# Kernel tuning notes

Measured on AMD Instinct MI355X. Metric: run time of the kernel, lower is better.

## Reference

```python
import jax, jax.numpy as jnp
import numpy as np

E = 250000          # num_edges
T = 1500000         # num_triplets
H = 128             # hidden_dim
NB = 8              # num_bilinear
NS = 7              # num_spherical
NR = 6              # num_radial
OUT = 128           # output_dim


def silu(x):
    return x * jax.nn.sigmoid(x)


def setup_inputs() -> dict:
    key = jax.random.key(0)
    ks = jax.random.split(key, 24)
    s = 1.0 / np.sqrt(H)
    inp = {
        "x": jax.random.normal(ks[0], (E, H), jnp.float32),
        "rbf": jax.random.uniform(ks[1], (E, NR), jnp.float32),
        "sbf": jax.random.uniform(ks[2], (T, NS * NR), jnp.float32),
        "idx_kj": jax.random.randint(ks[3], (T,), 0, E, jnp.int32),
        "idx_ji": jax.random.randint(ks[4], (T,), 0, E, jnp.int32),
        # weights stored [in, out] (math identical to torch y = x @ W.T + b)
        "lin_rbf_w": jax.random.normal(ks[5], (NR, H), jnp.float32) * (1.0 / np.sqrt(NR)),
        "lin_sbf_w": jax.random.normal(ks[6], (NS * NR, NB), jnp.float32) * (1.0 / np.sqrt(NS * NR)),
        "lin_kj_w": jax.random.normal(ks[7], (H, H), jnp.float32) * s,
        "lin_kj_b": jnp.zeros((H,), jnp.float32),
        "lin_ji_w": jax.random.normal(ks[8], (H, H), jnp.float32) * s,
        "lin_ji_b": jnp.zeros((H,), jnp.float32),
        "W": jax.random.normal(ks[9], (H, NB, H), jnp.float32) * (2.0 / H),
        "rb_w1": jax.random.normal(ks[10], (H, H), jnp.float32) * s,
        "rb_b1": jnp.zeros((H,), jnp.float32),
        "rb_w2": jax.random.normal(ks[11], (H, H), jnp.float32) * s,
        "rb_b2": jnp.zeros((H,), jnp.float32),
        "lin_w": jax.random.normal(ks[12], (H, H), jnp.float32) * s,
        "lin_b": jnp.zeros((H,), jnp.float32),
        "ra1_w1": jax.random.normal(ks[13], (H, H), jnp.float32) * s,
        "ra1_b1": jnp.zeros((H,), jnp.float32),
        "ra1_w2": jax.random.normal(ks[14], (H, H), jnp.float32) * s,
        "ra1_b2": jnp.zeros((H,), jnp.float32),
        "ra2_w1": jax.random.normal(ks[15], (H, H), jnp.float32) * s,
        "ra2_b1": jnp.zeros((H,), jnp.float32),
        "ra2_w2": jax.random.normal(ks[16], (H, H), jnp.float32) * s,
        "ra2_b2": jnp.zeros((H,), jnp.float32),
        "lin_out_w": jax.random.normal(ks[17], (H, OUT), jnp.float32) * s,
        "lin_out_b": jnp.zeros((OUT,), jnp.float32),
    }
    return inp


def _residual(h, w1, b1, w2, b2):
    return h + silu(silu(h @ w1 + b1) @ w2 + b2)


def reference(x, rbf, sbf, idx_kj, idx_ji,
              lin_rbf_w, lin_sbf_w, lin_kj_w, lin_kj_b, lin_ji_w, lin_ji_b, W,
              rb_w1, rb_b1, rb_w2, rb_b2, lin_w, lin_b,
              ra1_w1, ra1_b1, ra1_w2, ra1_b2, ra2_w1, ra2_b1, ra2_w2, ra2_b2,
              lin_out_w, lin_out_b):
    rbf_h = rbf @ lin_rbf_w                      # [E, H]
    sbf_h = sbf @ lin_sbf_w                      # [T, NB]
    x_ji = silu(x @ lin_ji_w + lin_ji_b)         # [E, H]
    x_kj = silu(x @ lin_kj_w + lin_kj_b) * rbf_h # [E, H]
    xk = x_kj[idx_kj]                            # gather -> [T, H]
    # trilinear einsum 'wj,wl,ijl->wi' without materializing [T, NB, H]:
    # loop over the small bilinear axis (NB=8), each step a [T,H]@[H,H] matmul
    out_t = jnp.zeros_like(xk)
    for j in range(NB):
        out_t = out_t + sbf_h[:, j:j + 1] * (xk @ W[:, j, :].T)   # [T, H]
    agg = jax.ops.segment_sum(out_t, idx_ji, num_segments=x.shape[0])  # [E, H]
    h = x_ji + agg
    h = _residual(h, rb_w1, rb_b1, rb_w2, rb_b2)
    h = silu(h @ lin_w + lin_b) + x
    h = _residual(h, ra1_w1, ra1_b1, ra1_w2, ra1_b2)
    h = _residual(h, ra2_w1, ra2_b1, ra2_w2, ra2_b2)
    return silu(h @ lin_out_w + lin_out_b)
```

## Files before the change

### kernel.cpp

```cpp
#include <hip/hip_runtime.h>

#define EDGES 250000
#define TRIP  1500000
#define HD    128
#define NBIL  8
#define NSR   42
#define NRAD  6

__device__ __forceinline__ float silu_f(float v) {
  return v / (1.0f + __expf(-v));
}

#define GET4(v,i) ((i)==0?(v).x:((i)==1?(v).y:((i)==2?(v).z:(v).w)))


__global__ void k_hist(const int* __restrict__ idxji, int* __restrict__ hist) {
  const int t = blockIdx.x * 256 + threadIdx.x;
  if (t < TRIP) atomicAdd(&hist[idxji[t]], 1);
}

__global__ __launch_bounds__(256) void k_scan1(const int* __restrict__ hist, int* __restrict__ blks) {
  __shared__ int sd[256];
  const int tid = threadIdx.x;
  const long base = (long)blockIdx.x * 1024 + tid * 4;
  int s = 0;
#pragma unroll
  for (int u = 0; u < 4; ++u) { const long i = base + u; if (i < EDGES) s += hist[i]; }
  sd[tid] = s; __syncthreads();
  for (int off = 128; off > 0; off >>= 1) { if (tid < off) sd[tid] += sd[tid + off]; __syncthreads(); }
  if (tid == 0) blks[blockIdx.x] = sd[0];
}

__global__ __launch_bounds__(256) void k_scan2(int* __restrict__ blks, int n) {
  __shared__ int sd[256];
  const int tid = threadIdx.x;
  const int v = (tid < n) ? blks[tid] : 0;
  sd[tid] = v; __syncthreads();
  for (int off = 1; off < 256; off <<= 1) {
    const int t = (tid >= off) ? sd[tid - off] : 0;
    __syncthreads();
    sd[tid] += t;
    __syncthreads();
  }
  if (tid < n) blks[tid] = sd[tid] - v;
}

__global__ __launch_bounds__(256) void k_scan3(int* __restrict__ cursor, const int* __restrict__ blks,
                                               int* __restrict__ offs) {
  __shared__ int sd[256];
  const int tid = threadIdx.x;
  const long base = (long)blockIdx.x * 1024 + tid * 4;
  int v[4]; int s = 0;
#pragma unroll
  for (int u = 0; u < 4; ++u) { const long i = base + u; v[u] = (i < EDGES) ? cursor[i] : 0; s += v[u]; }
  sd[tid] = s; __syncthreads();
  for (int off = 1; off < 256; off <<= 1) {
    const int tv = (tid >= off) ? sd[tid - off] : 0;
    __syncthreads();
    sd[tid] += tv;
    __syncthreads();
  }
  int run = blks[blockIdx.x] + sd[tid] - s;
#pragma unroll
  for (int u = 0; u < 4; ++u) {
    const long i = base + u;
    if (i < EDGES) { offs[i] = run; cursor[i] = run; }
    run += v[u];
  }
  if (blockIdx.x == 0 && tid == 0) offs[EDGES] = TRIP;
}

__global__ void k_scatter(const int* __restrict__ idxji, const int* __restrict__ idxkj,
                          int* __restrict__ cursor, int* __restrict__ gkj, int* __restrict__ tpos) {
  const int t = blockIdx.x * 256 + threadIdx.x;
  if (t < TRIP) {
    const int e = idxji[t];
    const int pos = atomicAdd(&cursor[e], 1);
    gkj[pos] = idxkj[t];
    tpos[t] = pos;
  }
}


__global__ void k_wt(const float* __restrict__ W, float* __restrict__ wt) {
  const int idx = blockIdx.x * 256 + threadIdx.x;
  if (idx < NBIL * HD * HD) {
    const int i = idx & (HD - 1);
    const int k = idx >> 7;
    const int j = k >> 7;
    const int l = k & (HD - 1);
    wt[idx] = W[((long)i * NBIL + j) * HD + l];
  }
}


__global__ __launch_bounds__(256) void k_sbfh(const float* __restrict__ sbf,
    const float* __restrict__ sw, const int* __restrict__ tpos, float* __restrict__ outp) {
  __shared__ float ss[256 * NSR];
  __shared__ float wls[NSR * NBIL];
  const int tid = threadIdx.x;
  const long t0 = (long)blockIdx.x * 256;
  const long gbase = t0 * NSR;
  for (int idx = tid; idx < 256 * NSR; idx += 256) {
    const long gi = gbase + idx;
    ss[idx] = (gi < (long)TRIP * NSR) ? sbf[gi] : 0.f;
  }
  for (int idx = tid; idx < NSR * NBIL; idx += 256) wls[idx] = sw[idx];
  __syncthreads();
  const long t = t0 + tid;
  if (t < TRIP) {
    float o[NBIL] = {};
    for (int r = 0; r < NSR; ++r) {
      const float sv = ss[tid * NSR + r];
#pragma unroll
      for (int j = 0; j < NBIL; ++j) o[j] += sv * wls[r * NBIL + j];
    }
    const long p = tpos[t];
    *(float4*)(outp + p * 8) = make_float4(o[0], o[1], o[2], o[3]);
    *(float4*)(outp + p * 8 + 4) = make_float4(o[4], o[5], o[6], o[7]);
  }
}


__global__ __launch_bounds__(256, 4) void k_edge(const float* __restrict__ x,
    const float* __restrict__ rbf, const float* __restrict__ rbfw,
    const float* __restrict__ wji, const float* __restrict__ bji,
    const float* __restrict__ wkj, const float* __restrict__ bkj,
    float* __restrict__ xji, float* __restrict__ xkj) {
  __shared__ float xs[32][HD + 4];
  __shared__ float rbfs[32][NRAD];
  __shared__ float rws[NRAD][HD];
  const int tid = threadIdx.x;
  const long e0 = (long)blockIdx.x * 32;
  for (int idx = tid; idx < 32 * (HD / 4); idx += 256) {
    const int el = idx >> 5; const int k4 = (idx & 31) << 2;
    const long e = e0 + el;
    float4 v = make_float4(0.f, 0.f, 0.f, 0.f);
    if (e < EDGES) v = *(const float4*)(x + e * HD + k4);
    *(float4*)&xs[el][k4] = v;
  }
  for (int idx = tid; idx < 32 * NRAD; idx += 256) {
    const int el = idx / NRAD, r = idx % NRAD;
    const long e = e0 + el;
    rbfs[el][r] = (e < EDGES) ? rbf[e * NRAD + r] : 0.f;
  }
  for (int idx = tid; idx < NRAD * HD; idx += 256) rws[idx / HD][idx % HD] = rbfw[idx];
  __syncthreads();
  const int cg = tid & 15, eg = tid >> 4;
  const int i0 = cg * 8;
  float aj[2][8] = {}, ak[2][8] = {};
  for (int k = 0; k < HD; k += 4) {
    const float4 xv0 = *(const float4*)&xs[eg * 2 + 0][k];
    const float4 xv1 = *(const float4*)&xs[eg * 2 + 1][k];
#pragma unroll
    for (int dk = 0; dk < 4; ++dk) {
      const float4 j0 = *(const float4*)(wji + (long)(k + dk) * HD + i0);
      const float4 j1 = *(const float4*)(wji + (long)(k + dk) * HD + i0 + 4);
      const float4 q0 = *(const float4*)(wkj + (long)(k + dk) * HD + i0);
      const float4 q1 = *(const float4*)(wkj + (long)(k + dk) * HD + i0 + 4);
      const float a0 = GET4(xv0, dk), a1 = GET4(xv1, dk);
#pragma unroll
      for (int c = 0; c < 4; ++c) {
        const float wja = GET4(j0, c), wjb = GET4(j1, c);
        const float wka = GET4(q0, c), wkb = GET4(q1, c);
        aj[0][c] += a0 * wja; aj[0][c + 4] += a0 * wjb;
        aj[1][c] += a1 * wja; aj[1][c + 4] += a1 * wjb;
        ak[0][c] += a0 * wka; ak[0][c + 4] += a0 * wkb;
        ak[1][c] += a1 * wka; ak[1][c + 4] += a1 * wkb;
      }
    }
  }
  const float4 bj0 = *(const float4*)(bji + i0), bj1 = *(const float4*)(bji + i0 + 4);
  const float4 bk0 = *(const float4*)(bkj + i0), bk1 = *(const float4*)(bkj + i0 + 4);
#pragma unroll
  for (int a = 0; a < 2; ++a) {
    const int el = eg * 2 + a;
    const long e = e0 + el;
    if (e >= EDGES) continue;
    float rh[8];
#pragma unroll
    for (int c = 0; c < 8; ++c) rh[c] = 0.f;
#pragma unroll
    for (int r = 0; r < NRAD; ++r) {
      const float rv = rbfs[el][r];
#pragma unroll
      for (int c = 0; c < 8; ++c) rh[c] += rv * rws[r][i0 + c];
    }
    float oj[8], ok[8];
#pragma unroll
    for (int c = 0; c < 4; ++c) {
      oj[c]     = silu_f(aj[a][c]     + GET4(bj0, c));
      oj[c + 4] = silu_f(aj[a][c + 4] + GET4(bj1, c));
      ok[c]     = silu_f(ak[a][c]     + GET4(bk0, c)) * rh[c];
      ok[c + 4] = silu_f(ak[a][c + 4] + GET4(bk1, c)) * rh[c + 4];
    }
    *(float4*)(xji + e * HD + i0)     = make_float4(oj[0], oj[1], oj[2], oj[3]);
    *(float4*)(xji + e * HD + i0 + 4) = make_float4(oj[4], oj[5], oj[6], oj[7]);
    *(float4*)(xkj + e * HD + i0)     = make_float4(ok[0], ok[1], ok[2], ok[3]);
    *(float4*)(xkj + e * HD + i0 + 4) = make_float4(ok[4], ok[5], ok[6], ok[7]);
  }
}


#define FMA16(sA, sB, xv) do { \
  m[0]  += (sA).x * (xv).x;  m[1]  += (sA).x * (xv).y; \
  m[2]  += (sA).y * (xv).x;  m[3]  += (sA).y * (xv).y; \
  m[4]  += (sA).z * (xv).x;  m[5]  += (sA).z * (xv).y; \
  m[6]  += (sA).w * (xv).x;  m[7]  += (sA).w * (xv).y; \
  m[8]  += (sB).x * (xv).x;  m[9]  += (sB).x * (xv).y; \
  m[10] += (sB).y * (xv).x;  m[11] += (sB).y * (xv).y; \
  m[12] += (sB).z * (xv).x;  m[13] += (sB).z * (xv).y; \
  m[14] += (sB).w * (xv).x;  m[15] += (sB).w * (xv).y; } while (0)

#define ACCUM_SEGMENT(t0, t1) \
    int t = (t0); \
    for (; t + 4 <= (t1); t += 4) { \
      const int g0 = gkj[t], g1 = gkj[t + 1], g2 = gkj[t + 2], g3 = gkj[t + 3]; \
      const float2 x0 = *(const float2*)(xkj + (long)g0 * HD + l2); \
      const float2 x1 = *(const float2*)(xkj + (long)g1 * HD + l2); \
      const float2 x2 = *(const float2*)(xkj + (long)g2 * HD + l2); \
      const float2 x3 = *(const float2*)(xkj + (long)g3 * HD + l2); \
      const float4 sa0 = *(const float4*)(sbfp + (long)t * 8); \
      const float4 sb0 = *(const float4*)(sbfp + (long)t * 8 + 4); \
      const float4 sa1 = *(const float4*)(sbfp + (long)(t + 1) * 8); \
      const float4 sb1 = *(const float4*)(sbfp + (long)(t + 1) * 8 + 4); \
      const float4 sa2 = *(const float4*)(sbfp + (long)(t + 2) * 8); \
      const float4 sb2 = *(const float4*)(sbfp + (long)(t + 2) * 8 + 4); \
      const float4 sa3 = *(const float4*)(sbfp + (long)(t + 3) * 8); \
      const float4 sb3 = *(const float4*)(sbfp + (long)(t + 3) * 8 + 4); \
      FMA16(sa0, sb0, x0); \
      FMA16(sa1, sb1, x1); \
      FMA16(sa2, sb2, x2); \
      FMA16(sa3, sb3, x3); \
    } \
    for (; t < (t1); ++t) { \
      const int g = gkj[t]; \
      const float2 xv = *(const float2*)(xkj + (long)g * HD + l2); \
      const float4 sa = *(const float4*)(sbfp + (long)t * 8); \
      const float4 sb = *(const float4*)(sbfp + (long)t * 8 + 4); \
      FMA16(sa, sb, xv); \
    }

__global__ __launch_bounds__(256, 4) void k_mA(const float* __restrict__ xkj,
    const float* __restrict__ sbfp, const int* __restrict__ gkj,
    const int* __restrict__ offs, float* __restrict__ M, int e0chunk, int ecount) {
  const int tid = threadIdx.x;
  const int lane = tid & 63;
  const int wv = tid >> 6;
  const int er = blockIdx.x * 4 + wv;
  if (er >= ecount) return;
  const long e = (long)e0chunk + er;
  const int l2 = lane * 2;
  float m[16];
#pragma unroll
  for (int q = 0; q < 16; ++q) m[q] = 0.f;
  const int t0 = offs[e], t1 = offs[e + 1];
  { ACCUM_SEGMENT(t0, t1) }
#pragma unroll
  for (int j = 0; j < 8; ++j)
    *(float2*)(M + (long)er * 1024 + j * 128 + l2) = make_float2(m[2 * j], m[2 * j + 1]);
}

__global__ __launch_bounds__(256, 4) void k_mB(const float* __restrict__ M,
    const float* __restrict__ wt, const float* __restrict__ xji,
    float* __restrict__ hout, int e0chunk, int ecount) {
  __shared__ float ms[64][68];
  const int tid = threadIdx.x;
  const int rbase = blockIdx.x * 64;
  const int cg = tid & 15, eg = tid >> 4;
  const int i0 = cg * 8;
  float acc[4][8] = {};
  for (int kc = 0; kc < 16; ++kc) {
    __syncthreads();
    for (int idx = tid; idx < 64 * 16; idx += 256) {
      const int r = idx >> 4, c4 = (idx & 15) << 2;
      const int row = rbase + r;
      float4 v = make_float4(0.f, 0.f, 0.f, 0.f);
      if (row < ecount) v = *(const float4*)(M + (long)row * 1024 + kc * 64 + c4);
      *(float4*)&ms[r][c4] = v;
    }
    __syncthreads();
    for (int kk = 0; kk < 64; kk += 4) {
      const float4 a0 = *(const float4*)&ms[eg * 4 + 0][kk];
      const float4 a1 = *(const float4*)&ms[eg * 4 + 1][kk];
      const float4 a2 = *(const float4*)&ms[eg * 4 + 2][kk];
      const float4 a3 = *(const float4*)&ms[eg * 4 + 3][kk];
#pragma unroll
      for (int dk = 0; dk < 4; ++dk) {
        const long kg = (long)kc * 64 + kk + dk;
        const float4 w0 = *(const float4*)(wt + kg * HD + i0);
        const float4 w1 = *(const float4*)(wt + kg * HD + i0 + 4);
        const float v0 = GET4(a0, dk), v1 = GET4(a1, dk), v2 = GET4(a2, dk), v3 = GET4(a3, dk);
#pragma unroll
        for (int c = 0; c < 4; ++c) {
          const float wa = GET4(w0, c), wb = GET4(w1, c);
          acc[0][c] += v0 * wa; acc[0][c + 4] += v0 * wb;
          acc[1][c] += v1 * wa; acc[1][c + 4] += v1 * wb;
          acc[2][c] += v2 * wa; acc[2][c + 4] += v2 * wb;
          acc[3][c] += v3 * wa; acc[3][c + 4] += v3 * wb;
        }
      }
    }
  }
#pragma unroll
  for (int a = 0; a < 4; ++a) {
    const int row = rbase + eg * 4 + a;
    if (row >= ecount) continue;
    const long e = (long)e0chunk + row;
    const float4 xa = *(const float4*)(xji + e * HD + i0);
    const float4 xb = *(const float4*)(xji + e * HD + i0 + 4);
    *(float4*)(hout + e * HD + i0)     = make_float4(acc[a][0] + xa.x, acc[a][1] + xa.y,
                                                     acc[a][2] + xa.z, acc[a][3] + xa.w);
    *(float4*)(hout + e * HD + i0 + 4) = make_float4(acc[a][4] + xb.x, acc[a][5] + xb.y,
                                                     acc[a][6] + xb.z, acc[a][7] + xb.w);
  }
}


__global__ __launch_bounds__(256, 2) void k_m(const float* __restrict__ xkj,
    const float* __restrict__ sbfp, const int* __restrict__ gkj,
    const int* __restrict__ offs, const float* __restrict__ wt,
    const float* __restrict__ xji, float* __restrict__ hout) {
  __shared__ float Mt[16][1024];
  const int tid = threadIdx.x;
  const int lane = tid & 63;
  const int wv = tid >> 6;
  const long e0 = (long)blockIdx.x * 16;
  const int l2 = lane * 2;
#pragma unroll 1
  for (int es = 0; es < 4; ++es) {
    const int el = wv * 4 + es;
    const long e = e0 + el;
    float m[16];
#pragma unroll
    for (int q = 0; q < 16; ++q) m[q] = 0.f;
    const int t0 = offs[e], t1 = offs[e + 1];
    { ACCUM_SEGMENT(t0, t1) }
#pragma unroll
    for (int j = 0; j < 8; ++j)
      *(float2*)&Mt[el][j * 128 + l2] = make_float2(m[2 * j], m[2 * j + 1]);
  }
  __syncthreads();
  const int cg = tid & 15, er = tid >> 4;
  const int i0 = cg * 8;
  float acc[8] = {};
  for (int kk = 0; kk < 1024; kk += 4) {
    const float4 mv = *(const float4*)&Mt[er][kk];
#pragma unroll
    for (int dk = 0; dk < 4; ++dk) {
      const float4 w0 = *(const float4*)(wt + (long)(kk + dk) * HD + i0);
      const float4 w1 = *(const float4*)(wt + (long)(kk + dk) * HD + i0 + 4);
      const float md = GET4(mv, dk);
      acc[0] += md * w0.x; acc[1] += md * w0.y; acc[2] += md * w0.z; acc[3] += md * w0.w;
      acc[4] += md * w1.x; acc[5] += md * w1.y; acc[6] += md * w1.z; acc[7] += md * w1.w;
    }
  }
  const long e = e0 + er;
  const float4 xa = *(const float4*)(xji + e * HD + i0);
  const float4 xb = *(const float4*)(xji + e * HD + i0 + 4);
  *(float4*)(hout + e * HD + i0)     = make_float4(acc[0] + xa.x, acc[1] + xa.y, acc[2] + xa.z, acc[3] + xa.w);
  *(float4*)(hout + e * HD + i0 + 4) = make_float4(acc[4] + xb.x, acc[5] + xb.y, acc[6] + xb.z, acc[7] + xb.w);
}


template<bool ADD>
__global__ __launch_bounds__(256, 4) void k_gemm(const float* __restrict__ in,
    const float* __restrict__ w, const float* __restrict__ bias,
    const float* __restrict__ addsrc, float* __restrict__ out) {
  __shared__ float xs[64][HD + 4];
  const int tid = threadIdx.x;
  const long e0 = (long)blockIdx.x * 64;
  for (int idx = tid; idx < 64 * (HD / 4); idx += 256) {
    const int el = idx >> 5; const int k4 = (idx & 31) << 2;
    const long e = e0 + el;
    float4 v = make_float4(0.f, 0.f, 0.f, 0.f);
    if (e < EDGES) v = *(const float4*)(in + e * HD + k4);
    *(float4*)&xs[el][k4] = v;
  }
  __syncthreads();
  const int cg = tid & 15, eg = tid >> 4;
  const int i0 = cg * 8;
  float acc[4][8] = {};
  for (int k = 0; k < HD; k += 4) {
    const float4 xv0 = *(const float4*)&xs[eg * 4 + 0][k];
    const float4 xv1 = *(const float4*)&xs[eg * 4 + 1][k];
    const float4 xv2 = *(const float4*)&xs[eg * 4 + 2][k];
    const float4 xv3 = *(const float4*)&xs[eg * 4 + 3][k];
#pragma unroll
    for (int dk = 0; dk < 4; ++dk) {
      const float4 w0 = *(const float4*)(w + (long)(k + dk) * HD + i0);
      const float4 w1 = *(const float4*)(w + (long)(k + dk) * HD + i0 + 4);
      const float a0 = GET4(xv0, dk), a1 = GET4(xv1, dk), a2 = GET4(xv2, dk), a3 = GET4(xv3, dk);
#pragma unroll
      for (int c = 0; c < 4; ++c) {
        const float wa = GET4(w0, c), wb = GET4(w1, c);
        acc[0][c] += a0 * wa; acc[0][c + 4] += a0 * wb;
        acc[1][c] += a1 * wa; acc[1][c + 4] += a1 * wb;
        acc[2][c] += a2 * wa; acc[2][c + 4] += a2 * wb;
        acc[3][c] += a3 * wa; acc[3][c + 4] += a3 * wb;
      }
    }
  }
  const float4 b0 = *(const float4*)(bias + i0);
  const float4 b1 = *(const float4*)(bias + i0 + 4);
#pragma unroll
  for (int a = 0; a < 4; ++a) {
    const long e = e0 + eg * 4 + a;
    if (e >= EDGES) continue;
    float o[8];
#pragma unroll
    for (int c = 0; c < 4; ++c) {
      o[c]     = silu_f(acc[a][c]     + GET4(b0, c));
      o[c + 4] = silu_f(acc[a][c + 4] + GET4(b1, c));
    }
    if (ADD) {
      const float4 ad0 = *(const float4*)(addsrc + e * HD + i0);
      const float4 ad1 = *(const float4*)(addsrc + e * HD + i0 + 4);
#pragma unroll
      for (int c = 0; c < 4; ++c) { o[c] += GET4(ad0, c); o[c + 4] += GET4(ad1, c); }
    }
    *(float4*)(out + e * HD + i0)     = make_float4(o[0], o[1], o[2], o[3]);
    *(float4*)(out + e * HD + i0 + 4) = make_float4(o[4], o[5], o[6], o[7]);
  }
}


__global__ __launch_bounds__(256, 2) void k_res(const float* __restrict__ in,
    const float* __restrict__ w1, const float* __restrict__ b1,
    const float* __restrict__ w2, const float* __restrict__ b2,
    float* __restrict__ out) {
  __shared__ float xs[64][HD + 4];
  __shared__ float ts[64][HD + 4];
  const int tid = threadIdx.x;
  const long e0 = (long)blockIdx.x * 64;
  for (int idx = tid; idx < 64 * (HD / 4); idx += 256) {
    const int el = idx >> 5; const int k4 = (idx & 31) << 2;
    const long e = e0 + el;
    float4 v = make_float4(0.f, 0.f, 0.f, 0.f);
    if (e < EDGES) v = *(const float4*)(in + e * HD + k4);
    *(float4*)&xs[el][k4] = v;
  }
  __syncthreads();
  const int cg = tid & 15, eg = tid >> 4;
  const int i0 = cg * 8;
  {
    float acc[4][8] = {};
    for (int k = 0; k < HD; k += 4) {
      const float4 xv0 = *(const float4*)&xs[eg * 4 + 0][k];
      const float4 xv1 = *(const float4*)&xs[eg * 4 + 1][k];
      const float4 xv2 = *(const float4*)&xs[eg * 4 + 2][k];
      const float4 xv3 = *(const float4*)&xs[eg * 4 + 3][k];
#pragma unroll
      for (int dk = 0; dk < 4; ++dk) {
        const float4 w0 = *(const float4*)(w1 + (long)(k + dk) * HD + i0);
        const float4 w1v = *(const float4*)(w1 + (long)(k + dk) * HD + i0 + 4);
        const float a0 = GET4(xv0, dk), a1 = GET4(xv1, dk), a2 = GET4(xv2, dk), a3 = GET4(xv3, dk);
#pragma unroll
        for (int c = 0; c < 4; ++c) {
          const float wa = GET4(w0, c), wb = GET4(w1v, c);
          acc[0][c] += a0 * wa; acc[0][c + 4] += a0 * wb;
          acc[1][c] += a1 * wa; acc[1][c + 4] += a1 * wb;
          acc[2][c] += a2 * wa; acc[2][c + 4] += a2 * wb;
          acc[3][c] += a3 * wa; acc[3][c + 4] += a3 * wb;
        }
      }
    }
    const float4 c0 = *(const float4*)(b1 + i0);
    const float4 c1 = *(const float4*)(b1 + i0 + 4);
#pragma unroll
    for (int a = 0; a < 4; ++a) {
      float o[8];
#pragma unroll
      for (int c = 0; c < 4; ++c) {
        o[c]     = silu_f(acc[a][c]     + GET4(c0, c));
        o[c + 4] = silu_f(acc[a][c + 4] + GET4(c1, c));
      }
      *(float4*)&ts[eg * 4 + a][i0]     = make_float4(o[0], o[1], o[2], o[3]);
      *(float4*)&ts[eg * 4 + a][i0 + 4] = make_float4(o[4], o[5], o[6], o[7]);
    }
  }
  __syncthreads();
  {
    float acc[4][8] = {};
    for (int k = 0; k < HD; k += 4) {
      const float4 xv0 = *(const float4*)&ts[eg * 4 + 0][k];
      const float4 xv1 = *(const float4*)&ts[eg * 4 + 1][k];
      const float4 xv2 = *(const float4*)&ts[eg * 4 + 2][k];
      const float4 xv3 = *(const float4*)&ts[eg * 4 + 3][k];
#pragma unroll
      for (int dk = 0; dk < 4; ++dk) {
        const float4 w0 = *(const float4*)(w2 + (long)(k + dk) * HD + i0);
        const float4 w1v = *(const float4*)(w2 + (long)(k + dk) * HD + i0 + 4);
        const float a0 = GET4(xv0, dk), a1 = GET4(xv1, dk), a2 = GET4(xv2, dk), a3 = GET4(xv3, dk);
#pragma unroll
        for (int c = 0; c < 4; ++c) {
          const float wa = GET4(w0, c), wb = GET4(w1v, c);
          acc[0][c] += a0 * wa; acc[0][c + 4] += a0 * wb;
          acc[1][c] += a1 * wa; acc[1][c + 4] += a1 * wb;
          acc[2][c] += a2 * wa; acc[2][c + 4] += a2 * wb;
          acc[3][c] += a3 * wa; acc[3][c + 4] += a3 * wb;
        }
      }
    }
    const float4 c0 = *(const float4*)(b2 + i0);
    const float4 c1 = *(const float4*)(b2 + i0 + 4);
#pragma unroll
    for (int a = 0; a < 4; ++a) {
      const long e = e0 + eg * 4 + a;
      if (e >= EDGES) continue;
      float o[8];
#pragma unroll
      for (int c = 0; c < 4; ++c) {
        o[c]     = silu_f(acc[a][c]     + GET4(c0, c)) + xs[eg * 4 + a][i0 + c];
        o[c + 4] = silu_f(acc[a][c + 4] + GET4(c1, c)) + xs[eg * 4 + a][i0 + 4 + c];
      }
      *(float4*)(out + e * HD + i0)     = make_float4(o[0], o[1], o[2], o[3]);
      *(float4*)(out + e * HD + i0 + 4) = make_float4(o[4], o[5], o[6], o[7]);
    }
  }
}


extern "C" void kernel_launch(void* const* d_in, const int* in_sizes, int n_in,
                              void* d_out, int out_size, void* d_ws, size_t ws_size,
                              hipStream_t stream) {
  const float* x         = (const float*)d_in[0];
  const float* rbf       = (const float*)d_in[1];
  const float* sbf       = (const float*)d_in[2];
  const int*   idx_kj    = (const int*)d_in[3];
  const int*   idx_ji    = (const int*)d_in[4];
  const float* lin_rbf_w = (const float*)d_in[5];
  const float* lin_sbf_w = (const float*)d_in[6];
  const float* lin_kj_w  = (const float*)d_in[7];
  const float* lin_kj_b  = (const float*)d_in[8];
  const float* lin_ji_w  = (const float*)d_in[9];
  const float* lin_ji_b  = (const float*)d_in[10];
  const float* Wtri      = (const float*)d_in[11];
  const float* rb_w1 = (const float*)d_in[12];
  const float* rb_b1 = (const float*)d_in[13];
  const float* rb_w2 = (const float*)d_in[14];
  const float* rb_b2 = (const float*)d_in[15];
  const float* lin_w = (const float*)d_in[16];
  const float* lin_b = (const float*)d_in[17];
  const float* ra1_w1 = (const float*)d_in[18];
  const float* ra1_b1 = (const float*)d_in[19];
  const float* ra1_w2 = (const float*)d_in[20];
  const float* ra1_b2 = (const float*)d_in[21];
  const float* ra2_w1 = (const float*)d_in[22];
  const float* ra2_b1 = (const float*)d_in[23];
  const float* ra2_w2 = (const float*)d_in[24];
  const float* ra2_b2 = (const float*)d_in[25];
  const float* lin_out_w = (const float*)d_in[26];
  const float* lin_out_b = (const float*)d_in[27];
  float* outp = (float*)d_out;

  const size_t EH = (size_t)EDGES * HD;
  float* buf0 = (float*)d_ws;
  float* buf1 = buf0 + EH;
  float* buf2 = buf1 + EH;
  float* sbfp = buf2 + EH;
  float* wt   = sbfp + (size_t)TRIP * NBIL;
  float* fend = wt + (size_t)NBIL * HD * HD;
  int* offs   = (int*)fend;
  int* cursor = offs + (EDGES + 4);
  int* gkj    = cursor + EDGES;
  int* tpos   = gkj + TRIP;
  int* blks   = tpos + TRIP;
  int* iend   = blks + 256;
  const size_t base_bytes = (size_t)((char*)iend - (char*)d_ws);
  const size_t moff = (base_bytes + 255) & ~(size_t)255;
  float* Mbuf = (float*)((char*)d_ws + moff);
  long ce = 0;
  if ((long)ws_size > (long)moff) {
    ce = ((long)ws_size - (long)moff) / (1024 * 4);
    ce &= ~63L;
    if (ce > 250048) ce = 250048;
  }
  const bool split = (ce >= 8192);

  hipMemsetAsync(cursor, 0, EDGES * sizeof(int), stream);
  const int TB  = (TRIP + 255) / 256;
  const int SCB = (EDGES + 1023) / 1024;
  k_hist<<<TB, 256, 0, stream>>>(idx_ji, cursor);
  k_scan1<<<SCB, 256, 0, stream>>>(cursor, blks);
  k_scan2<<<1, 256, 0, stream>>>(blks, SCB);
  k_scan3<<<SCB, 256, 0, stream>>>(cursor, blks, offs);
  k_scatter<<<TB, 256, 0, stream>>>(idx_ji, idx_kj, cursor, gkj, tpos);
  k_wt<<<(NBIL * HD * HD + 255) / 256, 256, 0, stream>>>(Wtri, wt);
  k_sbfh<<<TB, 256, 0, stream>>>(sbf, lin_sbf_w, tpos, sbfp);
  k_edge<<<(EDGES + 31) / 32, 256, 0, stream>>>(x, rbf, lin_rbf_w,
      lin_ji_w, lin_ji_b, lin_kj_w, lin_kj_b, buf0, buf1);

  if (split) {
    for (long c0 = 0; c0 < EDGES; c0 += ce) {
      const int ecount = (int)((EDGES - c0 < ce) ? (EDGES - c0) : ce);
      k_mA<<<(ecount + 3) / 4, 256, 0, stream>>>(buf1, sbfp, gkj, offs, Mbuf, (int)c0, ecount);
      k_mB<<<(ecount + 63) / 64, 256, 0, stream>>>(Mbuf, wt, buf0, buf2, (int)c0, ecount);
    }
  } else {
    k_m<<<EDGES / 16, 256, 0, stream>>>(buf1, sbfp, gkj, offs, wt, buf0, buf2);
  }

  const int GB = (EDGES + 63) / 64;
  k_res<<<GB, 256, 0, stream>>>(buf2, rb_w1, rb_b1, rb_w2, rb_b2, buf0);
  k_gemm<true ><<<GB, 256, 0, stream>>>(buf0, lin_w, lin_b, x, buf1);
  k_res<<<GB, 256, 0, stream>>>(buf1, ra1_w1, ra1_b1, ra1_w2, ra1_b2, buf2);
  k_res<<<GB, 256, 0, stream>>>(buf2, ra2_w1, ra2_b1, ra2_w2, ra2_b2, buf0);
  k_gemm<false><<<GB, 256, 0, stream>>>(buf0, lin_out_w, lin_out_b, nullptr, outp);
}
```

Before: 4.203 ms.

## Stage W tile in shared memory and enlarge k_mB tile to 128 rows

Reworks the M x W GEMM kernel so each block handles 128 edge rows with an 8x8 per-thread register tile. K-slices of 32 are staged for both M and the weight matrix in shared memory, where before weights were read directly from global memory for every FMA group. This aims to cut global weight traffic and raise arithmetic intensity per load. It costs more registers (64 accumulators) under the launch bound of 4 blocks per SM, and the chunk rounding moves to multiples of 128.

```diff
diff --git a/kernel.cpp b/kernel.cpp
--- a/kernel.cpp
+++ b/kernel.cpp
@@ -261,58 +261,71 @@
     *(float2*)(M + (long)er * 1024 + j * 128 + l2) = make_float2(m[2 * j], m[2 * j + 1]);
 }
 
+#define KC 32
+
 __global__ __launch_bounds__(256, 4) void k_mB(const float* __restrict__ M,
     const float* __restrict__ wt, const float* __restrict__ xji,
     float* __restrict__ hout, int e0chunk, int ecount) {
-  __shared__ float ms[64][68];
-  const int tid = threadIdx.x;
-  const int rbase = blockIdx.x * 64;
+  __shared__ float ms[128][KC + 4];
+  __shared__ float ws[KC][HD + 4];
+  const int tid = threadIdx.x;
+  const int rbase = blockIdx.x * 128;
   const int cg = tid & 15, eg = tid >> 4;
   const int i0 = cg * 8;
-  float acc[4][8] = {};
-  for (int kc = 0; kc < 16; ++kc) {
+  const int mc4 = (tid & 7) << 2;
+  const int mrow = tid >> 3;
+  const int wc4 = (tid & 31) << 2;
+  const int wkr = tid >> 5;
+  float acc[8][8] = {};
+  for (int kc = 0; kc < 1024; kc += KC) {
     __syncthreads();
-    for (int idx = tid; idx < 64 * 16; idx += 256) {
-      const int r = idx >> 4, c4 = (idx & 15) << 2;
-      const int row = rbase + r;
+#pragma unroll
+    for (int rr = 0; rr < 4; ++rr) {
+      const int r = mrow + rr * 32;
+      const int grow = rbase + r;
       float4 v = make_float4(0.f, 0.f, 0.f, 0.f);
-      if (row < ecount) v = *(const float4*)(M + (long)row * 1024 + kc * 64 + c4);
-      *(float4*)&ms[r][c4] = v;
+      if (grow < ecount) v = *(const float4*)(M + (long)grow * 1024 + kc + mc4);
+      *(float4*)&ms[r][mc4] = v;
+    }
+#pragma unroll
+    for (int kk = 0; kk < 4; ++kk) {
+      const int k = wkr * 4 + kk;
+      *(float4*)&ws[k][wc4] = *(const float4*)(wt + (long)(kc + k) * HD + wc4);
     }
     __syncthreads();
-    for (int kk = 0; kk < 64; kk += 4) {
-      const float4 a0 = *(const float4*)&ms[eg * 4 + 0][kk];
-      const float4 a1 = *(const float4*)&ms[eg * 4 + 1][kk];
-      const float4 a2 = *(const float4*)&ms[eg * 4 + 2][kk];
-      const float4 a3 = *(const float4*)&ms[eg * 4 + 3][kk];
+    for (int k4 = 0; k4 < KC; k4 += 4) {
+      float4 w[8];
 #pragma unroll
       for (int dk = 0; dk < 4; ++dk) {
-        const long kg = (long)kc * 64 + kk + dk;
-        const float4 w0 = *(const float4*)(wt + kg * HD + i0);
-        const float4 w1 = *(const float4*)(wt + kg * HD + i0 + 4);
-        const float v0 = GET4(a0, dk), v1 = GET4(a1, dk), v2 = GET4(a2, dk), v3 = GET4(a3, dk);
-#pragma unroll
-        for (int c = 0; c < 4; ++c) {
-          const float wa = GET4(w0, c), wb = GET4(w1, c);
-          acc[0][c] += v0 * wa; acc[0][c + 4] += v0 * wb;
-          acc[1][c] += v1 * wa; acc[1][c + 4] += v1 * wb;
-          acc[2][c] += v2 * wa; acc[2][c + 4] += v2 * wb;
-          acc[3][c] += v3 * wa; acc[3][c + 4] += v3 * wb;
+        w[2 * dk]     = *(const float4*)&ws[k4 + dk][i0];
+        w[2 * dk + 1] = *(const float4*)&ws[k4 + dk][i0 + 4];
+      }
+#pragma unroll
+      for (int ri = 0; ri < 8; ++ri) {
+        const float4 mv = *(const float4*)&ms[eg + 16 * ri][k4];
+#pragma unroll
+        for (int dk = 0; dk < 4; ++dk) {
+          const float a = GET4(mv, dk);
+          const float4 wa = w[2 * dk], wb = w[2 * dk + 1];
+          acc[ri][0] += a * wa.x; acc[ri][1] += a * wa.y;
+          acc[ri][2] += a * wa.z; acc[ri][3] += a * wa.w;
+          acc[ri][4] += a * wb.x; acc[ri][5] += a * wb.y;
+          acc[ri][6] += a * wb.z; acc[ri][7] += a * wb.w;
         }
       }
     }
   }
 #pragma unroll
-  for (int a = 0; a < 4; ++a) {
-    const int row = rbase + eg * 4 + a;
+  for (int ri = 0; ri < 8; ++ri) {
+    const int row = rbase + eg + 16 * ri;
     if (row >= ecount) continue;
     const long e = (long)e0chunk + row;
     const float4 xa = *(const float4*)(xji + e * HD + i0);
     const float4 xb = *(const float4*)(xji + e * HD + i0 + 4);
-    *(float4*)(hout + e * HD + i0)     = make_float4(acc[a][0] + xa.x, acc[a][1] + xa.y,
-                                                     acc[a][2] + xa.z, acc[a][3] + xa.w);
-    *(float4*)(hout + e * HD + i0 + 4) = make_float4(acc[a][4] + xb.x, acc[a][5] + xb.y,
-                                                     acc[a][6] + xb.z, acc[a][7] + xb.w);
+    *(float4*)(hout + e * HD + i0)     = make_float4(acc[ri][0] + xa.x, acc[ri][1] + xa.y,
+                                                     acc[ri][2] + xa.z, acc[ri][3] + xa.w);
+    *(float4*)(hout + e * HD + i0 + 4) = make_float4(acc[ri][4] + xb.x, acc[ri][5] + xb.y,
+                                                     acc[ri][6] + xb.z, acc[ri][7] + xb.w);
   }
 }
 
@@ -573,8 +586,8 @@
   long ce = 0;
   if ((long)ws_size > (long)moff) {
     ce = ((long)ws_size - (long)moff) / (1024 * 4);
-    ce &= ~63L;
-    if (ce > 250048) ce = 250048;
+    ce &= ~127L;
+    if (ce > 250112) ce = 250112;
   }
   const bool split = (ce >= 8192);
 
@@ -595,7 +608,7 @@
     for (long c0 = 0; c0 < EDGES; c0 += ce) {
       const int ecount = (int)((EDGES - c0 < ce) ? (EDGES - c0) : ce);
       k_mA<<<(ecount + 3) / 4, 256, 0, stream>>>(buf1, sbfp, gkj, offs, Mbuf, (int)c0, ecount);
-      k_mB<<<(ecount + 63) / 64, 256, 0, stream>>>(Mbuf, wt, buf0, buf2, (int)c0, ecount);
+      k_mB<<<(ecount + 127) / 128, 256, 0, stream>>>(Mbuf, wt, buf0, buf2, (int)c0, ecount);
     }
   } else {
     k_m<<<EDGES / 16, 256, 0, stream>>>(buf1, sbfp, gkj, offs, wt, buf0, buf2);
```

After: 3.978 ms. 1.06x faster.
